# Kernel optimization log

Measured on AMD Instinct MI355X. Metric: run time of the kernel, lower is better.

The kernel has to match this reference:

```python
import jax, jax.numpy as jnp
import numpy as np

N, D, B, C, T, TOD = 8192, 32, 2, 8, 12, 288
PARAM_SCALE = 0.3  # keep relu+softmax logits well-conditioned (original uses plain randn init)


def setup_inputs() -> dict:
    key = jax.random.key(0)
    k0, k1, k2, k3, k4 = jax.random.split(key, 5)
    return {
        "x": jax.random.normal(k0, (B, C, N, T), dtype=jnp.float32),
        "nodevec1": PARAM_SCALE * jax.random.normal(k1, (N, D), dtype=jnp.float32),
        "nodevec2": PARAM_SCALE * jax.random.normal(k2, (N, D), dtype=jnp.float32),
        "timevec": PARAM_SCALE * jax.random.normal(k3, (TOD, D), dtype=jnp.float32),
        "k": PARAM_SCALE * jax.random.normal(k4, (D, D, D), dtype=jnp.float32),
        "time_ind": 100,
    }


def reference(x, nodevec1, nodevec2, timevec, k, time_ind):
    # Dynamic Tucker-decomposition adjacency (SpatialGraphConv.forward, eval mode -> dropout is identity)
    tv = timevec[time_ind]                             # [D]   time_vec
    core = jnp.einsum('d,def->ef', tv, k)              # [D,D] adp1 (squeezed)
    # adp2/adp3 chain: (nodevec1 @ core) @ nodevec2.T  -> [N,N]
    adp = jnp.einsum('ne,ef->nf', nodevec1, core)      # [N,D]
    adp = jnp.einsum('nf,mf->nm', adp, nodevec2)       # [N,N]
    adp = jax.nn.softmax(jax.nn.relu(adp), axis=-1)    # row-softmax over neighbors
    # NConv: neighbor aggregation  'bcnt,nm->bcmt'
    return jnp.einsum('bcnt,nm->bcmt', x, adp)
```

## Files before the change

### kernel.cpp

```cpp
#include <hip/hip_runtime.h>
#include <hip/hip_bf16.h>


#define NN 8192
#define DD 32
#define TT 12
#define NSPLIT 8
#define CHUNK 1024
#define ESTR 72

typedef __attribute__((ext_vector_type(8))) short bf16x8;
typedef __attribute__((ext_vector_type(4))) short bf16x4;
typedef __attribute__((ext_vector_type(4))) float f32x4;

static __device__ __forceinline__ unsigned short f2bf(float f) {
  unsigned int u = __float_as_uint(f);
  u = (u + 0x7FFFu + ((u >> 16) & 1u)) >> 16;
  return (unsigned short)u;
}

static __device__ __forceinline__ float fexp2(float x) {
#if __has_builtin(__builtin_amdgcn_exp2f)
  return __builtin_amdgcn_exp2f(x);
#else
  return __builtin_exp2f(x);
#endif
}

__global__ __launch_bounds__(256) void k_prep(const float* __restrict__ nv1,
                                              const float* __restrict__ nv2,
                                              const float* __restrict__ timevec,
                                              const float* __restrict__ kk,
                                              const int* __restrict__ tind,
                                              unsigned short* __restrict__ t1b,
                                              unsigned short* __restrict__ nv2b,
                                              float* __restrict__ sums) {
  __shared__ float cs[1024];
  const int tid = threadIdx.x;
  if (tid < 128) sums[blockIdx.x * 128 + tid] = 0.f;
  const float* tv = timevec + (size_t)tind[0] * DD;
  for (int idx = tid; idx < 1024; idx += 256) {
    float acc = 0.f;
#pragma unroll
    for (int d = 0; d < DD; ++d) acc += tv[d] * kk[d * 1024 + idx];
    cs[idx] = acc;
  }
  __syncthreads();
  const int nbase = blockIdx.x * 128;
  const int f = tid & 31, sub = tid >> 5;
#pragma unroll 4
  for (int it = 0; it < 16; ++it) {
    const int n = nbase + it * 8 + sub;
    const float* nr = nv1 + (size_t)n * DD;
    float acc = 0.f;
#pragma unroll
    for (int e = 0; e < DD; ++e) acc += nr[e] * cs[e * DD + f];
    t1b[(size_t)n * DD + f] = f2bf(acc * 1.4426950408889634f);
  }
#pragma unroll 4
  for (int it = 0; it < 16; ++it) {
    const int idx = nbase * DD + it * 256 + tid;
    nv2b[idx] = f2bf(nv2[idx]);
  }
}

__global__ __launch_bounds__(256) void k_stats(const unsigned short* __restrict__ t1b,
                                               const unsigned short* __restrict__ nv2b,
                                               float* __restrict__ sums) {
  const int tid = threadIdx.x;
  const int w = tid >> 6, lane = tid & 63, q = lane >> 4, i16 = lane & 15;
  const int nbase = blockIdx.x * 64 + w * 16;
  bf16x8 a = *(const bf16x8*)(t1b + (size_t)(nbase + i16) * DD + q * 8);
  const f32x4 z4 = {0.f, 0.f, 0.f, 0.f};
  float s[4] = {0.f, 0.f, 0.f, 0.f};
  const int m0 = blockIdx.y * 1024;
  for (int mt = m0; mt < m0 + 1024; mt += 64) {
#pragma unroll
    for (int u = 0; u < 4; ++u) {
      bf16x8 b = *(const bf16x8*)(nv2b + (size_t)(mt + u * 16 + i16) * DD + q * 8);
      f32x4 d = __builtin_amdgcn_mfma_f32_16x16x32_bf16(a, b, z4, 0, 0, 0);
#pragma unroll
      for (int r = 0; r < 4; ++r) s[r] += fexp2(fmaxf(d[r], 0.f));
    }
  }
#pragma unroll
  for (int r = 0; r < 4; ++r)
    for (int off = 1; off < 16; off <<= 1) s[r] += __shfl_xor(s[r], off, 64);
  if (i16 == 0) {
#pragma unroll
    for (int r = 0; r < 4; ++r) atomicAdd(&sums[nbase + q * 4 + r], s[r]);
  }
}

__global__ __launch_bounds__(256) void k_y(const float* __restrict__ x,
                                           const float* __restrict__ sums,
                                           unsigned short* __restrict__ yT) {
  __shared__ float xs[3072];
  const int tid = threadIdx.x;
  const int n0 = blockIdx.x * 256;
  const int bc = blockIdx.y;
  const float* xp = x + (size_t)bc * NN * TT + (size_t)n0 * TT;
#pragma unroll
  for (int j = 0; j < 12; ++j) xs[j * 256 + tid] = xp[j * 256 + tid];
  __syncthreads();
  const float rinv = 1.0f / sums[n0 + tid];
#pragma unroll
  for (int t = 0; t < 12; ++t)
    yT[(size_t)(bc * TT + t) * NN + n0 + tid] = f2bf(xs[tid * 12 + t] * rinv);
}

__global__ __launch_bounds__(256, 4) void k_mega(const unsigned short* __restrict__ t1b,
                                                 const unsigned short* __restrict__ nv2b,
                                                 const unsigned short* __restrict__ yT,
                                                 float* __restrict__ part) {
  const int tid = threadIdx.x;
  const int w = tid >> 6, lane = tid & 63, q = lane >> 4, i16 = lane & 15;
  const int mb = blockIdx.x * 64;
  const int nt0 = blockIdx.y * CHUNK;

  __shared__ unsigned short Ew[2][64][ESTR];

  const bf16x8 bg = *(const bf16x8*)(nv2b + (size_t)(mb + w * 16 + i16) * DD + q * 8);
  const int rowm = w * 16 + i16;

  const f32x4 z4 = {0.f, 0.f, 0.f, 0.f};
  f32x4 acc[3][4];
#pragma unroll
  for (int c = 0; c < 3; ++c)
#pragma unroll
    for (int ms = 0; ms < 4; ++ms) acc[c][ms] = (f32x4){0.f, 0.f, 0.f, 0.f};

#pragma unroll
  for (int s = 0; s < 4; ++s) {
    bf16x8 at = *(const bf16x8*)(t1b + (size_t)(nt0 + s * 16 + i16) * DD + q * 8);
    f32x4 d = __builtin_amdgcn_mfma_f32_16x16x32_bf16(at, bg, z4, 0, 0, 0);
    bf16x4 e;
#pragma unroll
    for (int r = 0; r < 4; ++r) e[r] = (short)f2bf(fexp2(fmaxf(d[r], 0.f)));
    *(bf16x4*)&Ew[0][rowm][s * 16 + q * 4] = e;
  }
  __syncthreads();

  int p = 0;
  for (int st = 0; st < 16; ++st, p ^= 1) {
    const int nt = nt0 + st * 64;
    const bool more = (st < 15);

    bf16x8 atn[4];
    if (more) {
#pragma unroll
      for (int s = 0; s < 4; ++s)
        atn[s] = *(const bf16x8*)(t1b + (size_t)(nt + 64 + s * 16 + i16) * DD + q * 8);
    }

    bf16x8 yfr[3], efr[4];
#pragma unroll
    for (int c = 0; c < 3; ++c)
      yfr[c] = *(const bf16x8*)(yT + (size_t)((w * 3 + c) * 16 + i16) * NN + nt + q * 8);
#pragma unroll
    for (int ms = 0; ms < 4; ++ms)
      efr[ms] = *(const bf16x8*)&Ew[p][ms * 16 + i16][q * 8];

    f32x4 d0, d1;
    if (more) {
      d0 = __builtin_amdgcn_mfma_f32_16x16x32_bf16(atn[0], bg, z4, 0, 0, 0);
      d1 = __builtin_amdgcn_mfma_f32_16x16x32_bf16(atn[1], bg, z4, 0, 0, 0);
    }

#pragma unroll
    for (int c = 0; c < 3; ++c)
#pragma unroll
      for (int ms = 0; ms < 4; ++ms)
        acc[c][ms] = __builtin_amdgcn_mfma_f32_16x16x32_bf16(yfr[c], efr[ms], acc[c][ms], 0, 0, 0);

    if (more) {
      bf16x4 e0, e1;
#pragma unroll
      for (int r = 0; r < 4; ++r) {
        e0[r] = (short)f2bf(fexp2(fmaxf(d0[r], 0.f)));
        e1[r] = (short)f2bf(fexp2(fmaxf(d1[r], 0.f)));
      }
      *(bf16x4*)&Ew[p ^ 1][rowm][q * 4] = e0;
      *(bf16x4*)&Ew[p ^ 1][rowm][16 + q * 4] = e1;
      f32x4 d2 = __builtin_amdgcn_mfma_f32_16x16x32_bf16(atn[2], bg, z4, 0, 0, 0);
      f32x4 d3 = __builtin_amdgcn_mfma_f32_16x16x32_bf16(atn[3], bg, z4, 0, 0, 0);
      bf16x4 e2, e3;
#pragma unroll
      for (int r = 0; r < 4; ++r) {
        e2[r] = (short)f2bf(fexp2(fmaxf(d2[r], 0.f)));
        e3[r] = (short)f2bf(fexp2(fmaxf(d3[r], 0.f)));
      }
      *(bf16x4*)&Ew[p ^ 1][rowm][32 + q * 4] = e2;
      *(bf16x4*)&Ew[p ^ 1][rowm][48 + q * 4] = e3;
    }

#pragma unroll
    for (int c = 0; c < 3; ++c)
      yfr[c] = *(const bf16x8*)(yT + (size_t)((w * 3 + c) * 16 + i16) * NN + nt + 32 + q * 8);
#pragma unroll
    for (int ms = 0; ms < 4; ++ms)
      efr[ms] = *(const bf16x8*)&Ew[p][ms * 16 + i16][32 + q * 8];
#pragma unroll
    for (int c = 0; c < 3; ++c)
#pragma unroll
      for (int ms = 0; ms < 4; ++ms)
        acc[c][ms] = __builtin_amdgcn_mfma_f32_16x16x32_bf16(yfr[c], efr[ms], acc[c][ms], 0, 0, 0);

    __syncthreads();
  }

  float* pp = part + (size_t)blockIdx.y * 192 * NN;
#pragma unroll
  for (int c = 0; c < 3; ++c)
#pragma unroll
    for (int ms = 0; ms < 4; ++ms) {
      const int colbase = (w * 3 + c) * 16 + q * 4;
      const int m = mb + ms * 16 + i16;
#pragma unroll
      for (int r = 0; r < 4; ++r)
        pp[(size_t)(colbase + r) * NN + m] = acc[c][ms][r];
    }
}

__global__ __launch_bounds__(256) void k_reduce(const float* __restrict__ part,
                                                float* __restrict__ out) {
  __shared__ float os[3072];
  const int tid = threadIdx.x;
  const int m0 = blockIdx.x * 256;
  const int bc = blockIdx.y;
#pragma unroll
  for (int t = 0; t < 12; ++t) {
    const int col = bc * TT + t;
    float s = 0.f;
#pragma unroll
    for (int nc = 0; nc < NSPLIT; ++nc)
      s += part[((size_t)nc * 192 + col) * NN + m0 + tid];
    os[tid * 12 + t] = s;
  }
  __syncthreads();
  float* op = out + (size_t)bc * NN * TT + (size_t)m0 * TT;
#pragma unroll
  for (int j = 0; j < 12; ++j) op[j * 256 + tid] = os[j * 256 + tid];
}

extern "C" void kernel_launch(void* const* d_in, const int* in_sizes, int n_in,
                              void* d_out, int out_size, void* d_ws, size_t ws_size,
                              hipStream_t stream) {
  const float* x = (const float*)d_in[0];
  const float* nv1 = (const float*)d_in[1];
  const float* nv2 = (const float*)d_in[2];
  const float* tv = (const float*)d_in[3];
  const float* kk = (const float*)d_in[4];
  const int* tind = (const int*)d_in[5];
  float* out = (float*)d_out;

  char* ws = (char*)d_ws;
  unsigned short* t1b  = (unsigned short*)(ws);
  unsigned short* nv2b = (unsigned short*)(ws + 524288);
  float* sums          = (float*)(ws + 1048576);
  unsigned short* yT   = (unsigned short*)(ws + 1081344);
  float* part          = (float*)(ws + 4227072);

  k_prep<<<64, 256, 0, stream>>>(nv1, nv2, tv, kk, tind, t1b, nv2b, sums);
  k_stats<<<dim3(128, 8), 256, 0, stream>>>(t1b, nv2b, sums);
  k_y<<<dim3(32, 16), 256, 0, stream>>>(x, sums, yT);
  k_mega<<<dim3(128, NSPLIT), 256, 0, stream>>>(t1b, nv2b, yT, part);
  k_reduce<<<dim3(32, 16), 256, 0, stream>>>(part, out);
}
```

Before: 178.8 us.

## Prefetch stats loads, pad LDS transposes, and use lightweight barriers in main kernel

The stats kernel now software-prefetches the next four nv2 fragments while computing the current ones, so global-load latency is hidden behind the MFMA and exp work. The transpose buffers in the y and reduce kernels are padded from stride 12 to 13 to avoid LDS bank conflicts on the strided accesses. The main kernel replaces __syncthreads with a barrier that waits only on LDS counters, so outstanding global prefetches are not drained at each step. The cost is extra index arithmetic (div/mod by 12) and slightly more LDS and registers.

```diff
diff --git a/kernel.cpp b/kernel.cpp
--- a/kernel.cpp
+++ b/kernel.cpp
@@ -26,6 +26,13 @@
   return __builtin_exp2f(x);
 #endif
 }
+
+#define RAWBAR()                                          \
+  do {                                                    \
+    asm volatile("s_waitcnt lgkmcnt(0)" ::: "memory");    \
+    __builtin_amdgcn_sched_barrier(0);                    \
+    __builtin_amdgcn_s_barrier();                         \
+  } while (0)
 
 __global__ __launch_bounds__(256) void k_prep(const float* __restrict__ nv1,
                                               const float* __restrict__ nv2,
@@ -74,15 +81,27 @@
   const f32x4 z4 = {0.f, 0.f, 0.f, 0.f};
   float s[4] = {0.f, 0.f, 0.f, 0.f};
   const int m0 = blockIdx.y * 1024;
+#define LDB(mt, u) (*(const bf16x8*)(nv2b + (size_t)((mt) + (u)*16 + i16) * DD + q * 8))
+  bf16x8 b0 = LDB(m0, 0), b1 = LDB(m0, 1), b2 = LDB(m0, 2), b3 = LDB(m0, 3);
   for (int mt = m0; mt < m0 + 1024; mt += 64) {
-#pragma unroll
-    for (int u = 0; u < 4; ++u) {
-      bf16x8 b = *(const bf16x8*)(nv2b + (size_t)(mt + u * 16 + i16) * DD + q * 8);
-      f32x4 d = __builtin_amdgcn_mfma_f32_16x16x32_bf16(a, b, z4, 0, 0, 0);
-#pragma unroll
-      for (int r = 0; r < 4; ++r) s[r] += fexp2(fmaxf(d[r], 0.f));
-    }
-  }
+    const int mtn = (mt + 64 < m0 + 1024) ? (mt + 64) : mt;
+    bf16x8 n0 = LDB(mtn, 0), n1 = LDB(mtn, 1), n2 = LDB(mtn, 2), n3 = LDB(mtn, 3);
+    f32x4 d;
+    d = __builtin_amdgcn_mfma_f32_16x16x32_bf16(a, b0, z4, 0, 0, 0);
+#pragma unroll
+    for (int r = 0; r < 4; ++r) s[r] += fexp2(fmaxf(d[r], 0.f));
+    d = __builtin_amdgcn_mfma_f32_16x16x32_bf16(a, b1, z4, 0, 0, 0);
+#pragma unroll
+    for (int r = 0; r < 4; ++r) s[r] += fexp2(fmaxf(d[r], 0.f));
+    d = __builtin_amdgcn_mfma_f32_16x16x32_bf16(a, b2, z4, 0, 0, 0);
+#pragma unroll
+    for (int r = 0; r < 4; ++r) s[r] += fexp2(fmaxf(d[r], 0.f));
+    d = __builtin_amdgcn_mfma_f32_16x16x32_bf16(a, b3, z4, 0, 0, 0);
+#pragma unroll
+    for (int r = 0; r < 4; ++r) s[r] += fexp2(fmaxf(d[r], 0.f));
+    b0 = n0; b1 = n1; b2 = n2; b3 = n3;
+  }
+#undef LDB
 #pragma unroll
   for (int r = 0; r < 4; ++r)
     for (int off = 1; off < 16; off <<= 1) s[r] += __shfl_xor(s[r], off, 64);
@@ -95,18 +114,21 @@
 __global__ __launch_bounds__(256) void k_y(const float* __restrict__ x,
                                            const float* __restrict__ sums,
                                            unsigned short* __restrict__ yT) {
-  __shared__ float xs[3072];
+  __shared__ float xs[3328];
   const int tid = threadIdx.x;
   const int n0 = blockIdx.x * 256;
   const int bc = blockIdx.y;
   const float* xp = x + (size_t)bc * NN * TT + (size_t)n0 * TT;
 #pragma unroll
-  for (int j = 0; j < 12; ++j) xs[j * 256 + tid] = xp[j * 256 + tid];
+  for (int j = 0; j < 12; ++j) {
+    const int idx = j * 256 + tid;
+    xs[(idx / 12) * 13 + idx % 12] = xp[idx];
+  }
   __syncthreads();
   const float rinv = 1.0f / sums[n0 + tid];
 #pragma unroll
   for (int t = 0; t < 12; ++t)
-    yT[(size_t)(bc * TT + t) * NN + n0 + tid] = f2bf(xs[tid * 12 + t] * rinv);
+    yT[(size_t)(bc * TT + t) * NN + n0 + tid] = f2bf(xs[tid * 13 + t] * rinv);
 }
 
 __global__ __launch_bounds__(256, 4) void k_mega(const unsigned short* __restrict__ t1b,
@@ -139,7 +161,7 @@
     for (int r = 0; r < 4; ++r) e[r] = (short)f2bf(fexp2(fmaxf(d[r], 0.f)));
     *(bf16x4*)&Ew[0][rowm][s * 16 + q * 4] = e;
   }
-  __syncthreads();
+  RAWBAR();
 
   int p = 0;
   for (int st = 0; st < 16; ++st, p ^= 1) {
@@ -206,7 +228,7 @@
       for (int ms = 0; ms < 4; ++ms)
         acc[c][ms] = __builtin_amdgcn_mfma_f32_16x16x32_bf16(yfr[c], efr[ms], acc[c][ms], 0, 0, 0);
 
-    __syncthreads();
+    RAWBAR();
   }
 
   float* pp = part + (size_t)blockIdx.y * 192 * NN;
@@ -224,7 +246,7 @@
 
 __global__ __launch_bounds__(256) void k_reduce(const float* __restrict__ part,
                                                 float* __restrict__ out) {
-  __shared__ float os[3072];
+  __shared__ float os[3328];
   const int tid = threadIdx.x;
   const int m0 = blockIdx.x * 256;
   const int bc = blockIdx.y;
@@ -235,12 +257,15 @@
 #pragma unroll
     for (int nc = 0; nc < NSPLIT; ++nc)
       s += part[((size_t)nc * 192 + col) * NN + m0 + tid];
-    os[tid * 12 + t] = s;
+    os[tid * 13 + t] = s;
   }
   __syncthreads();
   float* op = out + (size_t)bc * NN * TT + (size_t)m0 * TT;
 #pragma unroll
-  for (int j = 0; j < 12; ++j) op[j * 256 + tid] = os[j * 256 + tid];
+  for (int j = 0; j < 12; ++j) {
+    const int idx = j * 256 + tid;
+    op[idx] = os[(idx / 12) * 13 + idx % 12];
+  }
 }
 
 extern "C" void kernel_launch(void* const* d_in, const int* in_sizes, int n_in,
```

Measured after the change: 177.7 us. No clear change (-0.6%).
